# Performance work log

Measured on AMD Instinct MI355X. Metric: run time of the kernel, lower is better.

The kernel has to match this reference:

```python
import jax, jax.numpy as jnp
import numpy as np

N_NODES, N_EDGES = 100000, 800000
F_NODE, F_EDGE, N_CLASSES = 128, 16, 10


def _lin(key, fan_in, fan_out, bias=True):
    k1, k2 = jax.random.split(key)
    W = jax.random.normal(k1, (fan_in, fan_out), jnp.float32) * 0.05
    if bias:
        b = jax.random.normal(k2, (fan_out,), jnp.float32) * 0.05
        return W, b
    return (W,)


def setup_inputs() -> dict:
    key = jax.random.key(0)
    ks = jax.random.split(key, 24)
    inp = {
        "x": jax.random.normal(ks[0], (N_NODES, F_NODE), jnp.float32),
        "edge_index": jax.random.randint(ks[1], (2, N_EDGES), 0, N_NODES, jnp.int64 if jax.config.jax_enable_x64 else jnp.int32),
        "edge_attr": jax.random.normal(ks[2], (N_EDGES, F_EDGE), jnp.float32),
    }
    dims = [(F_NODE, 128), (128, 128), (128, 256)]  # (in_channels, out_channels) per layer
    i = 3
    for li, (din, dout) in enumerate(dims, start=1):
        inp[f"Wq{li}"], inp[f"bq{li}"] = _lin(ks[i], din, dout); i += 1
        inp[f"Wk{li}"], inp[f"bk{li}"] = _lin(ks[i], din, dout); i += 1
        inp[f"Wv{li}"], inp[f"bv{li}"] = _lin(ks[i], din, dout); i += 1
        (inp[f"We{li}"],) = _lin(ks[i], F_EDGE, dout, bias=False); i += 1  # PyG lin_edge: bias=False
        inp[f"Ws{li}"], inp[f"bs{li}"] = _lin(ks[i], din, dout); i += 1  # root/skip weight
    inp["Wc"], inp["bc"] = _lin(ks[i], 256, N_CLASSES)
    return inp


def transformer_conv(x, src, dst, edge_attr, Wq, bq, Wk, bk, Wv, bv, We, Ws, bs):
    """PyG TransformerConv, heads=1, concat=True, root_weight=True."""
    N = x.shape[0]
    C = Wq.shape[1]
    q = x @ Wq + bq                      # [N, C]
    k = x @ Wk + bk                      # [N, C]
    v = x @ Wv + bv                      # [N, C]
    e = edge_attr @ We                   # [E, C] edge-conditioned term
    # per-edge attention logits: <q_i, k_j + e_ij> / sqrt(C)
    alpha = jnp.sum(q[dst] * (k[src] + e), axis=-1) / jnp.sqrt(jnp.float32(C))  # [E]
    # segment softmax over edges sharing a destination node
    m = jax.ops.segment_max(alpha, dst, num_segments=N)
    p = jnp.exp(alpha - m[dst])
    s = jax.ops.segment_sum(p, dst, num_segments=N)
    a = p / (s[dst] + 1e-16)
    # scatter-aggregate weighted messages (value_j + edge term)
    out = jax.ops.segment_sum(a[:, None] * (v[src] + e), dst, num_segments=N)  # [N, C]
    return out + x @ Ws + bs             # root/skip connection


def reference(x, edge_index, edge_attr,
              Wq1, bq1, Wk1, bk1, Wv1, bv1, We1, Ws1, bs1,
              Wq2, bq2, Wk2, bk2, Wv2, bv2, We2, Ws2, bs2,
              Wq3, bq3, Wk3, bk3, Wv3, bv3, We3, Ws3, bs3,
              Wc, bc):
    src, dst = edge_index[0], edge_index[1]
    h = transformer_conv(x, src, dst, edge_attr, Wq1, bq1, Wk1, bk1, Wv1, bv1, We1, Ws1, bs1)
    h = jax.nn.relu(h)  # dropout is identity in eval mode
    h = transformer_conv(h, src, dst, edge_attr, Wq2, bq2, Wk2, bk2, Wv2, bv2, We2, Ws2, bs2)
    h = jax.nn.relu(h)
    h = transformer_conv(h, src, dst, edge_attr, Wq3, bq3, Wk3, bk3, Wv3, bv3, We3, Ws3, bs3)
    return h @ Wc + bc                   # [N, num_classes]
```

## Files before the change

### kernel.cpp

```cpp
#include <hip/hip_runtime.h>
#include <math.h>


typedef unsigned int uint;
typedef unsigned short ushort;
typedef _Float16 f16x8 __attribute__((ext_vector_type(8)));
typedef _Float16 h16x2 __attribute__((ext_vector_type(2)));
typedef float f32x4 __attribute__((ext_vector_type(4)));
typedef float f32x2 __attribute__((ext_vector_type(2)));

__device__ __forceinline__ ushort f2h(float f) {
    return __builtin_bit_cast(ushort, (_Float16)f);
}
__device__ __forceinline__ float h2f(ushort h) {
    return (float)__builtin_bit_cast(_Float16, h);
}
__device__ __forceinline__ h16x2 bch2(uint u) { return __builtin_bit_cast(h16x2, u); }
__device__ __forceinline__ f32x2 cvt2(uint u) {
    h16x2 h = bch2(u);
    return (f32x2){(float)h.x, (float)h.y};
}

#if __has_builtin(__builtin_amdgcn_fdot2)
#define FDOT2(a, b, c) __builtin_amdgcn_fdot2((a), (b), (c), false)
#else
__device__ __forceinline__ float fdot2_sw(h16x2 a, h16x2 b, float c) {
    return fmaf((float)a.x, (float)b.x, fmaf((float)a.y, (float)b.y, c));
}
#define FDOT2(a, b, c) fdot2_sw((a), (b), (c))
#endif

__global__ void k_zero(uint* p, int n) {
    int i = blockIdx.x * 256 + threadIdx.x;
    if (i < n) p[i] = 0u;
}

__global__ void k_hist(const int* __restrict__ dst, uint* __restrict__ counts, int E, int N) {
    int e = blockIdx.x * 256 + threadIdx.x;
    if (e < E) {
        int d = dst[e];
        d = (d < 0) ? 0 : (d >= N ? N - 1 : d);
        atomicAdd(&counts[d], 1u);
    }
}

__global__ void k_scan1(const uint* __restrict__ counts, uint* __restrict__ bsum, int n) {
    __shared__ uint sm[256];
    int tid = threadIdx.x;
    int base = blockIdx.x * 1024 + tid * 4;
    uint s = 0;
#pragma unroll
    for (int j = 0; j < 4; ++j)
        if (base + j < n) s += counts[base + j];
    sm[tid] = s;
    __syncthreads();
    for (int d = 128; d > 0; d >>= 1) {
        if (tid < d) sm[tid] += sm[tid + d];
        __syncthreads();
    }
    if (tid == 0) bsum[blockIdx.x] = sm[0];
}

__global__ void k_scan2(uint* bsum, int nb) {
    if (threadIdx.x == 0 && blockIdx.x == 0) {
        uint run = 0;
        for (int i = 0; i < nb; ++i) { uint v = bsum[i]; bsum[i] = run; run += v; }
    }
}

__global__ void k_scan3(const uint* __restrict__ counts, const uint* __restrict__ bsum,
                        uint* __restrict__ row_ptr, int n, int E) {
    __shared__ uint sm[256];
    int tid = threadIdx.x;
    int base = blockIdx.x * 1024 + tid * 4;
    uint local[4];
    uint s = 0;
#pragma unroll
    for (int j = 0; j < 4; ++j) {
        local[j] = (base + j < n) ? counts[base + j] : 0u;
        s += local[j];
    }
    sm[tid] = s;
    __syncthreads();
    for (int d = 1; d < 256; d <<= 1) {
        uint v = (tid >= d) ? sm[tid - d] : 0u;
        __syncthreads();
        sm[tid] += v;
        __syncthreads();
    }
    uint run = sm[tid] - s + bsum[blockIdx.x];
#pragma unroll
    for (int j = 0; j < 4; ++j)
        if (base + j < n) { row_ptr[base + j] = run; run += local[j]; }
    if (blockIdx.x == 0 && tid == 0) row_ptr[n] = (uint)E;
}

__global__ void k_fill(const int* __restrict__ ei, const uint* __restrict__ row_ptr,
                       uint* __restrict__ cursor, int2* __restrict__ srcid, int E, int N) {
    int e = blockIdx.x * 256 + threadIdx.x;
    if (e >= E) return;
    int s = ei[e];
    int d = ei[E + e];
    s = (s < 0) ? 0 : (s >= N ? N - 1 : s);
    d = (d < 0) ? 0 : (d >= N ? N - 1 : d);
    uint idx = row_ptr[d] + atomicAdd(&cursor[d], 1u);
    srcid[idx] = make_int2(s, e);
}

__global__ void k_cvt(const float4* __restrict__ in, ushort4* __restrict__ outp, int n4) {
    int i = blockIdx.x * 256 + threadIdx.x;
    if (i >= n4) return;
    float4 v = in[i];
    ushort4 o;
    o.x = f2h(v.x); o.y = f2h(v.y); o.z = f2h(v.z); o.w = f2h(v.w);
    outp[i] = o;
}

__global__ void k_packg(const float* __restrict__ Wq, const float* __restrict__ bq,
                        const float* __restrict__ We, float* __restrict__ Wgf,
                        float* __restrict__ bgf, int C) {
    int id = blockIdx.x * 256 + threadIdx.x;
    if (id < 2048) {
        int k = id >> 4, f = id & 15;
        float s = 0.f;
        for (int c = 0; c < C; ++c) s = fmaf(Wq[k * C + c], We[f * C + c], s);
        Wgf[id] = s;
    } else if (id < 2064) {
        int f = id - 2048;
        float s = 0.f;
        for (int c = 0; c < C; ++c) s = fmaf(bq[c], We[f * C + c], s);
        bgf[f] = s;
    }
}

__global__ void k_packw(const float* __restrict__ Wq, const float* __restrict__ Wk,
                        const float* __restrict__ Wv, const float* __restrict__ Ws,
                        const float* __restrict__ Wgf, ushort* __restrict__ Bp, int C) {
    int nct = (4 * C + 16) >> 4;
    int total = 4 * nct * 512;
    int id = blockIdx.x * 256 + threadIdx.x;
    if (id >= total) return;
    int j = id & 7;
    int rest = id >> 3;
    int lane = rest & 63;
    rest >>= 6;
    int ct = rest % nct;
    int kt = rest / nct;
    int k = kt * 32 + ((lane >> 4) << 3) + j;
    int c = (ct << 4) + (lane & 15);
    float w;
    if (c < 4 * C) {
        int mat = c / C, cc = c % C;
        const float* W = (mat == 0) ? Wq : (mat == 1) ? Wk : (mat == 2) ? Wv : Ws;
        w = W[k * C + cc];
    } else {
        w = Wgf[k * 16 + (c - 4 * C)];
    }
    Bp[id] = f2h(w);
}

__global__ void k_bias(const float* __restrict__ bq, const float* __restrict__ bk,
                       const float* __restrict__ bv, const float* __restrict__ bs,
                       const float* __restrict__ bgf, float* __restrict__ outp, int C) {
    int c = blockIdx.x * 256 + threadIdx.x;
    if (c >= 4 * C + 16) return;
    float v;
    if (c < 4 * C) {
        int mat = c / C, cc = c % C;
        const float* b = (mat == 0) ? bq : (mat == 1) ? bk : (mat == 2) ? bv : bs;
        v = b[cc];
    } else {
        v = bgf[c - 4 * C];
    }
    outp[c] = v;
}

__global__ __launch_bounds__(256) void k_gemm(const ushort* __restrict__ A,
                                              const ushort* __restrict__ Bp,
                                              const float* __restrict__ bias,
                                              ushort* __restrict__ H,
                                              ushort* __restrict__ S,
                                              ushort* __restrict__ g, int C) {
    int fourC = 4 * C, threeC = 3 * C;
    int P = fourC + 16;
    int nct = P >> 4;
    int lane = threadIdx.x & 63;
    int wave = threadIdx.x >> 6;
    int quad = lane >> 4;
    int r = lane & 15;
    int m0 = blockIdx.y << 4;
    int c0 = (blockIdx.x << 8) + (wave << 6);
    int ct0 = c0 >> 4;
    if (ct0 >= nct) return;
    int row = m0 + r;

    f32x4 acc[4];
#pragma unroll
    for (int i = 0; i < 4; ++i) acc[i] = (f32x4){0.f, 0.f, 0.f, 0.f};

#pragma unroll
    for (int kk = 0; kk < 4; ++kk) {
        f16x8 a = *(const f16x8*)(A + (size_t)row * 128 + kk * 32 + (quad << 3));
#pragma unroll
        for (int i = 0; i < 4; ++i) {
            if (ct0 + i < nct) {
                f16x8 b = *(const f16x8*)(Bp + ((size_t)((kk * nct + ct0 + i) << 6) + lane) * 8);
                acc[i] = __builtin_amdgcn_mfma_f32_16x16x32_f16(a, b, acc[i], 0, 0, 0);
            }
        }
    }
#pragma unroll
    for (int i = 0; i < 4; ++i) {
        int cc = c0 + (i << 4) + r;
        if (cc >= P) continue;
        float bi = bias[cc];
#pragma unroll
        for (int reg = 0; reg < 4; ++reg) {
            int rr = m0 + (quad << 2) + reg;
            ushort val = f2h(acc[i][reg] + bi);
            if (cc < threeC)      H[(size_t)rr * threeC + cc] = val;
            else if (cc < fourC)  S[(size_t)rr * C + (cc - threeC)] = val;
            else                  g[(size_t)rr * 16 + (cc - fourC)] = val;
        }
    }
}

template <int C, int GSIZE, bool RELU>
__global__ __launch_bounds__(256, 6) void k_edge(const ushort* __restrict__ H,
                                                 ushort* __restrict__ S,
                                                 const ushort* __restrict__ g,
                                                 const uint* __restrict__ row_ptr,
                                                 const int2* __restrict__ srcid,
                                                 const float* __restrict__ eattr,
                                                 const float* __restrict__ We,
                                                 int N) {
    constexpr int VR = C / GSIZE;
    constexpr int TH = 3 * C;
    constexpr int GPB = 256 / GSIZE;
    __shared__ float swex[GPB][17];
    const float scale = (C == 128) ? 0.08838834764831843f : 0.0625f;
    const float foldk = 16.0f / (float)GSIZE;

    int lane = threadIdx.x & (GSIZE - 1);
    int grp = threadIdx.x / GSIZE;
    int f = lane & 15;
    int node = blockIdx.x * GPB + grp;
    if (node >= N) return;
    int lvr = lane * VR;

    uint4 qv = *(const uint4*)(H + (size_t)node * TH + lvr);
    h16x2 q0 = bch2(qv.x), q1 = bch2(qv.y), q2 = bch2(qv.z), q3 = bch2(qv.w);
    float gl = h2f(g[(size_t)node * 16 + f]);
    float fg = foldk * gl;
    uint beg = row_ptr[node], end = row_ptr[node + 1];

    float l = 0.f, w = 0.f;
    f32x2 acc[4];
#pragma unroll
    for (int j = 0; j < 4; ++j) acc[j] = (f32x2){0.f, 0.f};

    for (uint t = beg; t < end; t += 4) {
        uint t1 = (t + 1 < end) ? t + 1 : t;
        uint t2 = (t + 2 < end) ? t + 2 : t;
        uint t3 = (t + 3 < end) ? t + 3 : t;
        int2 s0 = srcid[t], s1 = srcid[t1], s2 = srcid[t2], s3 = srcid[t3];
        float at0 = eattr[(size_t)s0.y * 16 + f];
        float at1 = eattr[(size_t)s1.y * 16 + f];
        float at2 = eattr[(size_t)s2.y * 16 + f];
        float at3 = eattr[(size_t)s3.y * 16 + f];
        const ushort* hb0 = H + (size_t)s0.x * TH + C + lvr;
        const ushort* hb1 = H + (size_t)s1.x * TH + C + lvr;
        const ushort* hb2 = H + (size_t)s2.x * TH + C + lvr;
        const ushort* hb3 = H + (size_t)s3.x * TH + C + lvr;
        uint4 k0 = *(const uint4*)hb0, v0 = *(const uint4*)(hb0 + C);
        uint4 k1 = *(const uint4*)hb1, v1 = *(const uint4*)(hb1 + C);
        uint4 k2 = *(const uint4*)hb2, v2 = *(const uint4*)(hb2 + C);
        uint4 k3 = *(const uint4*)hb3, v3 = *(const uint4*)(hb3 + C);

        float p0 = at0 * fg, p1 = at1 * fg, p2 = at2 * fg, p3 = at3 * fg;
        p0 = FDOT2(q0, bch2(k0.x), p0); p0 = FDOT2(q1, bch2(k0.y), p0);
        p0 = FDOT2(q2, bch2(k0.z), p0); p0 = FDOT2(q3, bch2(k0.w), p0);
        p1 = FDOT2(q0, bch2(k1.x), p1); p1 = FDOT2(q1, bch2(k1.y), p1);
        p1 = FDOT2(q2, bch2(k1.z), p1); p1 = FDOT2(q3, bch2(k1.w), p1);
        p2 = FDOT2(q0, bch2(k2.x), p2); p2 = FDOT2(q1, bch2(k2.y), p2);
        p2 = FDOT2(q2, bch2(k2.z), p2); p2 = FDOT2(q3, bch2(k2.w), p2);
        p3 = FDOT2(q0, bch2(k3.x), p3); p3 = FDOT2(q1, bch2(k3.y), p3);
        p3 = FDOT2(q2, bch2(k3.z), p3); p3 = FDOT2(q3, bch2(k3.w), p3);

        p0 += __shfl_xor(p0, 1); p1 += __shfl_xor(p1, 1);
        p2 += __shfl_xor(p2, 1); p3 += __shfl_xor(p3, 1);
        p0 += __shfl_xor(p0, 2); p1 += __shfl_xor(p1, 2);
        p2 += __shfl_xor(p2, 2); p3 += __shfl_xor(p3, 2);
        p0 += __shfl_xor(p0, 4); p1 += __shfl_xor(p1, 4);
        p2 += __shfl_xor(p2, 4); p3 += __shfl_xor(p3, 4);
        p0 += __shfl_xor(p0, 8); p1 += __shfl_xor(p1, 8);
        p2 += __shfl_xor(p2, 8); p3 += __shfl_xor(p3, 8);
        if (GSIZE == 32) {
            p0 += __shfl_xor(p0, 16); p1 += __shfl_xor(p1, 16);
            p2 += __shfl_xor(p2, 16); p3 += __shfl_xor(p3, 16);
        }
        float e0 = __expf(p0 * scale);
        float e1 = (t + 1 < end) ? __expf(p1 * scale) : 0.f;
        float e2 = (t + 2 < end) ? __expf(p2 * scale) : 0.f;
        float e3 = (t + 3 < end) ? __expf(p3 * scale) : 0.f;
        l += (e0 + e1) + (e2 + e3);
        w = fmaf(e0, at0, w); w = fmaf(e1, at1, w);
        w = fmaf(e2, at2, w); w = fmaf(e3, at3, w);
        f32x2 eb;
        eb = (f32x2){e0, e0};
        acc[0] = __builtin_elementwise_fma(cvt2(v0.x), eb, acc[0]);
        acc[1] = __builtin_elementwise_fma(cvt2(v0.y), eb, acc[1]);
        acc[2] = __builtin_elementwise_fma(cvt2(v0.z), eb, acc[2]);
        acc[3] = __builtin_elementwise_fma(cvt2(v0.w), eb, acc[3]);
        eb = (f32x2){e1, e1};
        acc[0] = __builtin_elementwise_fma(cvt2(v1.x), eb, acc[0]);
        acc[1] = __builtin_elementwise_fma(cvt2(v1.y), eb, acc[1]);
        acc[2] = __builtin_elementwise_fma(cvt2(v1.z), eb, acc[2]);
        acc[3] = __builtin_elementwise_fma(cvt2(v1.w), eb, acc[3]);
        eb = (f32x2){e2, e2};
        acc[0] = __builtin_elementwise_fma(cvt2(v2.x), eb, acc[0]);
        acc[1] = __builtin_elementwise_fma(cvt2(v2.y), eb, acc[1]);
        acc[2] = __builtin_elementwise_fma(cvt2(v2.z), eb, acc[2]);
        acc[3] = __builtin_elementwise_fma(cvt2(v2.w), eb, acc[3]);
        eb = (f32x2){e3, e3};
        acc[0] = __builtin_elementwise_fma(cvt2(v3.x), eb, acc[0]);
        acc[1] = __builtin_elementwise_fma(cvt2(v3.y), eb, acc[1]);
        acc[2] = __builtin_elementwise_fma(cvt2(v3.z), eb, acc[2]);
        acc[3] = __builtin_elementwise_fma(cvt2(v3.w), eb, acc[3]);
    }

    float inv = 1.f / (l + 1e-16f);
    if (lane < 16) swex[grp][lane] = w;
    f32x2 ew[4];
#pragma unroll
    for (int j = 0; j < 4; ++j) ew[j] = (f32x2){0.f, 0.f};
#pragma unroll
    for (int f2i = 0; f2i < 16; ++f2i) {
        float wfs = swex[grp][f2i];
        f32x2 wf = (f32x2){wfs, wfs};
        const f32x4* wrow = (const f32x4*)(We + f2i * C + lvr);
        f32x4 c0 = wrow[0], c1 = wrow[1];
        ew[0] = __builtin_elementwise_fma(c0.lo, wf, ew[0]);
        ew[1] = __builtin_elementwise_fma(c0.hi, wf, ew[1]);
        ew[2] = __builtin_elementwise_fma(c1.lo, wf, ew[2]);
        ew[3] = __builtin_elementwise_fma(c1.hi, wf, ew[3]);
    }
    ushort* srow = S + (size_t)node * C + lvr;
    uint4 skv = *(const uint4*)srow;
    const uint* sp = (const uint*)&skv;
    uint4 ov;
    uint* op = (uint*)&ov;
#pragma unroll
    for (int hh = 0; hh < 4; ++hh) {
        f32x2 sk = cvt2(sp[hh]);
        float o0 = (acc[hh].x + ew[hh].x) * inv + sk.x;
        float o1 = (acc[hh].y + ew[hh].y) * inv + sk.y;
        if (RELU) { o0 = fmaxf(o0, 0.f); o1 = fmaxf(o1, 0.f); }
        op[hh] = (uint)f2h(o0) | ((uint)f2h(o1) << 16);
    }
    *(uint4*)srow = ov;
}

__global__ void k_cls(const ushort* __restrict__ h, const float* __restrict__ Wc,
                      const float* __restrict__ bc, float* __restrict__ outp, int N) {
    int t = blockIdx.x * 256 + threadIdx.x;
    int node = t >> 4;
    int c = t & 15;
    if (node >= N || c >= 10) return;
    const ushort* hr = h + (size_t)node * 256;
    float acc = 0.f;
#pragma unroll 4
    for (int k4 = 0; k4 < 64; ++k4) {
        uint2 u = *(const uint2*)(hr + k4 * 4);
        f32x2 a01 = cvt2(u.x);
        f32x2 a23 = cvt2(u.y);
        int kb = k4 * 4;
        acc = fmaf(a01.x, Wc[(kb + 0) * 10 + c], acc);
        acc = fmaf(a01.y, Wc[(kb + 1) * 10 + c], acc);
        acc = fmaf(a23.x, Wc[(kb + 2) * 10 + c], acc);
        acc = fmaf(a23.y, Wc[(kb + 3) * 10 + c], acc);
    }
    outp[node * 10 + c] = acc + bc[c];
}

extern "C" void kernel_launch(void* const* d_in, const int* in_sizes, int n_in,
                              void* d_out, int out_size, void* d_ws, size_t ws_size,
                              hipStream_t stream) {
    const float* x = (const float*)d_in[0];
    const int* ei = (const int*)d_in[1];
    const float* eattr = (const float*)d_in[2];
    const int N = in_sizes[0] / 128;
    const int E = in_sizes[1] / 2;

    const float* Wq[3], *bq[3], *Wk[3], *bk[3], *Wv[3], *bv[3], *We[3], *Ws[3], *bs[3];
    for (int li = 0; li < 3; ++li) {
        int base = 3 + li * 9;
        Wq[li] = (const float*)d_in[base + 0];
        bq[li] = (const float*)d_in[base + 1];
        Wk[li] = (const float*)d_in[base + 2];
        bk[li] = (const float*)d_in[base + 3];
        Wv[li] = (const float*)d_in[base + 4];
        bv[li] = (const float*)d_in[base + 5];
        We[li] = (const float*)d_in[base + 6];
        Ws[li] = (const float*)d_in[base + 7];
        bs[li] = (const float*)d_in[base + 8];
    }
    const float* Wc = (const float*)d_in[30];
    const float* bc = (const float*)d_in[31];

    size_t off = 0;
    char* base = (char*)d_ws;
    auto alloc = [&](size_t bytes) -> void* {
        void* p = base + off;
        off = (off + bytes + 255) & ~(size_t)255;
        return p;
    };
    ushort* SA = (ushort*)alloc((size_t)N * 256 * 2);
    ushort* SB = (ushort*)alloc((size_t)N * 128 * 2);
    ushort* H  = (ushort*)alloc((size_t)N * 768 * 2);
    ushort* gbuf = (ushort*)alloc((size_t)N * 16 * 2);
    ushort* Bp = (ushort*)alloc(140000 * 2);
    float* biasc = (float*)alloc(1040 * 4);
    float* Wgf = (float*)alloc(2048 * 4);
    float* bgf = (float*)alloc(16 * 4);
    uint* row_ptr = (uint*)alloc((size_t)(N + 1) * 4);
    uint* counts = (uint*)alloc((size_t)N * 4);
    uint* cursor = (uint*)alloc((size_t)N * 4);
    uint* bsum = (uint*)alloc(1024 * 4);
    int2* srcid = (int2*)alloc((size_t)E * 8);

    ushort* xb = SB;

    int nb = (N + 1023) / 1024;

    k_zero<<<(N + 255) / 256, 256, 0, stream>>>(counts, N);
    k_zero<<<(N + 255) / 256, 256, 0, stream>>>(cursor, N);
    k_hist<<<(E + 255) / 256, 256, 0, stream>>>(ei + E, counts, E, N);
    k_scan1<<<nb, 256, 0, stream>>>(counts, bsum, N);
    k_scan2<<<1, 64, 0, stream>>>(bsum, nb);
    k_scan3<<<nb, 256, 0, stream>>>(counts, bsum, row_ptr, N, E);
    k_fill<<<(E + 255) / 256, 256, 0, stream>>>(ei, row_ptr, cursor, srcid, E, N);

    int n4 = N * 128 / 4;
    k_cvt<<<(n4 + 255) / 256, 256, 0, stream>>>((const float4*)x, (ushort4*)xb, n4);

    for (int li = 0; li < 3; ++li) {
        int C = (li == 2) ? 256 : 128;
        int P = 4 * C + 16;
        int packTotal = 4 * (P >> 4) * 512;
        const ushort* A = (li == 0) ? xb : (li == 1) ? SA : SB;
        ushort* Sout = (li == 1) ? SB : SA;

        k_packg<<<9, 256, 0, stream>>>(Wq[li], bq[li], We[li], Wgf, bgf, C);
        k_packw<<<(packTotal + 255) / 256, 256, 0, stream>>>(Wq[li], Wk[li], Wv[li], Ws[li], Wgf, Bp, C);
        k_bias<<<(P + 255) / 256, 256, 0, stream>>>(bq[li], bk[li], bv[li], bs[li], bgf, biasc, C);
        k_gemm<<<dim3((P + 255) / 256, N / 16), 256, 0, stream>>>(A, Bp, biasc, H, Sout, gbuf, C);
        if (li == 2)
            k_edge<256, 32, false><<<(N * 32 + 255) / 256, 256, 0, stream>>>(H, Sout, gbuf, row_ptr, srcid, eattr, We[li], N);
        else
            k_edge<128, 16, true><<<(N * 16 + 255) / 256, 256, 0, stream>>>(H, Sout, gbuf, row_ptr, srcid, eattr, We[li], N);
    }

    k_cls<<<(N * 16 + 255) / 256, 256, 0, stream>>>(SA, Wc, bc, (float*)d_out, N);
}
```

Before: 1.027 ms.

## Split fused edge kernel into logit/exp pass and value aggregation pass

The single per-node edge kernel becomes two passes. The first gathers K rows, computes the exponentiated attention weights, and writes them to an fp16 per-edge buffer along with the per-node denominator and edge-attr weighted sums. The second pass gathers only V rows, accumulates the weighted values and applies the edge and skip terms. The aim is to cut register pressure and per-iteration gather volume in each kernel, at the cost of an extra launch, a second index traversal, extra global traffic for the new buffers, and fp16 rounding of the weights.

```diff
diff --git a/kernel.cpp b/kernel.cpp
--- a/kernel.cpp
+++ b/kernel.cpp
@@ -225,19 +225,17 @@
     }
 }
 
-template <int C, int GSIZE, bool RELU>
-__global__ __launch_bounds__(256, 6) void k_edge(const ushort* __restrict__ H,
-                                                 ushort* __restrict__ S,
-                                                 const ushort* __restrict__ g,
-                                                 const uint* __restrict__ row_ptr,
-                                                 const int2* __restrict__ srcid,
-                                                 const float* __restrict__ eattr,
-                                                 const float* __restrict__ We,
-                                                 int N) {
+template <int C, int GSIZE>
+__global__ __launch_bounds__(256, 6) void k_edge1(const ushort* __restrict__ H,
+                                                  ushort* g,
+                                                  const uint* __restrict__ row_ptr,
+                                                  const int2* __restrict__ srcid,
+                                                  const float* __restrict__ eattr,
+                                                  ushort* __restrict__ ebuf,
+                                                  float* __restrict__ lbuf, int N) {
     constexpr int VR = C / GSIZE;
     constexpr int TH = 3 * C;
     constexpr int GPB = 256 / GSIZE;
-    __shared__ float swex[GPB][17];
     const float scale = (C == 128) ? 0.08838834764831843f : 0.0625f;
     const float foldk = 16.0f / (float)GSIZE;
 
@@ -250,32 +248,23 @@
 
     uint4 qv = *(const uint4*)(H + (size_t)node * TH + lvr);
     h16x2 q0 = bch2(qv.x), q1 = bch2(qv.y), q2 = bch2(qv.z), q3 = bch2(qv.w);
-    float gl = h2f(g[(size_t)node * 16 + f]);
-    float fg = foldk * gl;
+    float fg = foldk * h2f(g[(size_t)node * 16 + f]);
     uint beg = row_ptr[node], end = row_ptr[node + 1];
 
     float l = 0.f, w = 0.f;
-    f32x2 acc[4];
-#pragma unroll
-    for (int j = 0; j < 4; ++j) acc[j] = (f32x2){0.f, 0.f};
-
     for (uint t = beg; t < end; t += 4) {
         uint t1 = (t + 1 < end) ? t + 1 : t;
         uint t2 = (t + 2 < end) ? t + 2 : t;
         uint t3 = (t + 3 < end) ? t + 3 : t;
-        int2 s0 = srcid[t], s1 = srcid[t1], s2 = srcid[t2], s3 = srcid[t3];
-        float at0 = eattr[(size_t)s0.y * 16 + f];
-        float at1 = eattr[(size_t)s1.y * 16 + f];
-        float at2 = eattr[(size_t)s2.y * 16 + f];
-        float at3 = eattr[(size_t)s3.y * 16 + f];
-        const ushort* hb0 = H + (size_t)s0.x * TH + C + lvr;
-        const ushort* hb1 = H + (size_t)s1.x * TH + C + lvr;
-        const ushort* hb2 = H + (size_t)s2.x * TH + C + lvr;
-        const ushort* hb3 = H + (size_t)s3.x * TH + C + lvr;
-        uint4 k0 = *(const uint4*)hb0, v0 = *(const uint4*)(hb0 + C);
-        uint4 k1 = *(const uint4*)hb1, v1 = *(const uint4*)(hb1 + C);
-        uint4 k2 = *(const uint4*)hb2, v2 = *(const uint4*)(hb2 + C);
-        uint4 k3 = *(const uint4*)hb3, v3 = *(const uint4*)(hb3 + C);
+        int2 se0 = srcid[t], se1 = srcid[t1], se2 = srcid[t2], se3 = srcid[t3];
+        float at0 = eattr[(size_t)se0.y * 16 + f];
+        float at1 = eattr[(size_t)se1.y * 16 + f];
+        float at2 = eattr[(size_t)se2.y * 16 + f];
+        float at3 = eattr[(size_t)se3.y * 16 + f];
+        uint4 k0 = *(const uint4*)(H + (size_t)se0.x * TH + C + lvr);
+        uint4 k1 = *(const uint4*)(H + (size_t)se1.x * TH + C + lvr);
+        uint4 k2 = *(const uint4*)(H + (size_t)se2.x * TH + C + lvr);
+        uint4 k3 = *(const uint4*)(H + (size_t)se3.x * TH + C + lvr);
 
         float p0 = at0 * fg, p1 = at1 * fg, p2 = at2 * fg, p3 = at3 * fg;
         p0 = FDOT2(q0, bch2(k0.x), p0); p0 = FDOT2(q1, bch2(k0.y), p0);
@@ -306,6 +295,61 @@
         l += (e0 + e1) + (e2 + e3);
         w = fmaf(e0, at0, w); w = fmaf(e1, at1, w);
         w = fmaf(e2, at2, w); w = fmaf(e3, at3, w);
+        if (lane < 4) {
+            uint tj = t + lane;
+            if (tj < end) {
+                float ee = (lane == 0) ? e0 : (lane == 1) ? e1 : (lane == 2) ? e2 : e3;
+                ebuf[tj] = f2h(ee);
+            }
+        }
+    }
+    if (lane < 16) g[(size_t)node * 16 + lane] = f2h(w);
+    if (lane == 0) lbuf[node] = l;
+}
+
+template <int C, int GSIZE, bool RELU>
+__global__ __launch_bounds__(256, 6) void k_edge2(const ushort* __restrict__ H,
+                                                  ushort* __restrict__ S,
+                                                  const uint* __restrict__ row_ptr,
+                                                  const int2* __restrict__ srcid,
+                                                  const ushort* __restrict__ ebuf,
+                                                  const ushort* __restrict__ wbuf,
+                                                  const float* __restrict__ lbuf,
+                                                  const float* __restrict__ We, int N) {
+    constexpr int VR = C / GSIZE;
+    constexpr int TH = 3 * C;
+    constexpr int GPB = 256 / GSIZE;
+    __shared__ float swex[GPB][17];
+
+    int lane = threadIdx.x & (GSIZE - 1);
+    int grp = threadIdx.x / GSIZE;
+    int node = blockIdx.x * GPB + grp;
+    if (node >= N) return;
+    int lvr = lane * VR;
+    uint beg = row_ptr[node], end = row_ptr[node + 1];
+
+    ushort* srow = S + (size_t)node * C + lvr;
+    uint4 skv = *(const uint4*)srow;
+    if (lane < 16) swex[grp][lane] = h2f(wbuf[(size_t)node * 16 + lane]);
+    float l = lbuf[node];
+
+    f32x2 acc[4];
+#pragma unroll
+    for (int j = 0; j < 4; ++j) acc[j] = (f32x2){0.f, 0.f};
+
+    for (uint t = beg; t < end; t += 4) {
+        uint t1 = (t + 1 < end) ? t + 1 : t;
+        uint t2 = (t + 2 < end) ? t + 2 : t;
+        uint t3 = (t + 3 < end) ? t + 3 : t;
+        int s0 = srcid[t].x, s1 = srcid[t1].x, s2 = srcid[t2].x, s3 = srcid[t3].x;
+        float e0 = h2f(ebuf[t]);
+        float e1 = (t + 1 < end) ? h2f(ebuf[t1]) : 0.f;
+        float e2 = (t + 2 < end) ? h2f(ebuf[t2]) : 0.f;
+        float e3 = (t + 3 < end) ? h2f(ebuf[t3]) : 0.f;
+        uint4 v0 = *(const uint4*)(H + (size_t)s0 * TH + 2 * C + lvr);
+        uint4 v1 = *(const uint4*)(H + (size_t)s1 * TH + 2 * C + lvr);
+        uint4 v2 = *(const uint4*)(H + (size_t)s2 * TH + 2 * C + lvr);
+        uint4 v3 = *(const uint4*)(H + (size_t)s3 * TH + 2 * C + lvr);
         f32x2 eb;
         eb = (f32x2){e0, e0};
         acc[0] = __builtin_elementwise_fma(cvt2(v0.x), eb, acc[0]);
@@ -330,7 +374,6 @@
     }
 
     float inv = 1.f / (l + 1e-16f);
-    if (lane < 16) swex[grp][lane] = w;
     f32x2 ew[4];
 #pragma unroll
     for (int j = 0; j < 4; ++j) ew[j] = (f32x2){0.f, 0.f};
@@ -345,8 +388,6 @@
         ew[2] = __builtin_elementwise_fma(c1.lo, wf, ew[2]);
         ew[3] = __builtin_elementwise_fma(c1.hi, wf, ew[3]);
     }
-    ushort* srow = S + (size_t)node * C + lvr;
-    uint4 skv = *(const uint4*)srow;
     const uint* sp = (const uint*)&skv;
     uint4 ov;
     uint* op = (uint*)&ov;
@@ -428,8 +469,10 @@
     uint* cursor = (uint*)alloc((size_t)N * 4);
     uint* bsum = (uint*)alloc(1024 * 4);
     int2* srcid = (int2*)alloc((size_t)E * 8);
+    ushort* ebuf = (ushort*)alloc((size_t)E * 2);
 
     ushort* xb = SB;
+    float* lbuf = (float*)counts;
 
     int nb = (N + 1023) / 1024;
 
@@ -455,10 +498,13 @@
         k_packw<<<(packTotal + 255) / 256, 256, 0, stream>>>(Wq[li], Wk[li], Wv[li], Ws[li], Wgf, Bp, C);
         k_bias<<<(P + 255) / 256, 256, 0, stream>>>(bq[li], bk[li], bv[li], bs[li], bgf, biasc, C);
         k_gemm<<<dim3((P + 255) / 256, N / 16), 256, 0, stream>>>(A, Bp, biasc, H, Sout, gbuf, C);
-        if (li == 2)
-            k_edge<256, 32, false><<<(N * 32 + 255) / 256, 256, 0, stream>>>(H, Sout, gbuf, row_ptr, srcid, eattr, We[li], N);
-        else
-            k_edge<128, 16, true><<<(N * 16 + 255) / 256, 256, 0, stream>>>(H, Sout, gbuf, row_ptr, srcid, eattr, We[li], N);
+        if (li == 2) {
+            k_edge1<256, 32><<<(N * 32 + 255) / 256, 256, 0, stream>>>(H, gbuf, row_ptr, srcid, eattr, ebuf, lbuf, N);
+            k_edge2<256, 32, false><<<(N * 32 + 255) / 256, 256, 0, stream>>>(H, Sout, row_ptr, srcid, ebuf, gbuf, lbuf, We[li], N);
+        } else {
+            k_edge1<128, 16><<<(N * 16 + 255) / 256, 256, 0, stream>>>(H, gbuf, row_ptr, srcid, eattr, ebuf, lbuf, N);
+            k_edge2<128, 16, true><<<(N * 16 + 255) / 256, 256, 0, stream>>>(H, Sout, row_ptr, srcid, ebuf, gbuf, lbuf, We[li], N);
+        }
     }
 
     k_cls<<<(N * 16 + 255) / 256, 256, 0, stream>>>(SA, Wc, bc, (float*)d_out, N);
```

After: 1.054 ms. +2.7%, slower.

## Keep GEMM B fragments in registers across row tiles; unroll edge loop by two

Applied to the files above, without the earlier changes.

The GEMM kernel now loads each wave's B-weight fragments into registers once, then loops over eight 16-row tiles per block, so fewer weight fetches are repeated per block. The grid shrinks by eight in y and launch bounds request four blocks per SM. Separately, the edge aggregation loop processes two edges per iteration instead of four. This lowers register pressure and tail waste, at the cost of fewer gathers in flight to hide latency.

```diff
diff --git a/kernel.cpp b/kernel.cpp
--- a/kernel.cpp
+++ b/kernel.cpp
@@ -175,12 +175,14 @@
     outp[c] = v;
 }
 
-__global__ __launch_bounds__(256) void k_gemm(const ushort* __restrict__ A,
-                                              const ushort* __restrict__ Bp,
-                                              const float* __restrict__ bias,
-                                              ushort* __restrict__ H,
-                                              ushort* __restrict__ S,
-                                              ushort* __restrict__ g, int C) {
+__global__ __launch_bounds__(256, 4) void k_gemm(const ushort* __restrict__ A,
+                                                 const ushort* __restrict__ Bp,
+                                                 const float* __restrict__ bias,
+                                                 ushort* __restrict__ H,
+                                                 ushort* __restrict__ S,
+                                                 ushort* __restrict__ g,
+                                                 int C, int mt_total) {
+    constexpr int RT = 8;
     int fourC = 4 * C, threeC = 3 * C;
     int P = fourC + 16;
     int nct = P >> 4;
@@ -188,39 +190,61 @@
     int wave = threadIdx.x >> 6;
     int quad = lane >> 4;
     int r = lane & 15;
-    int m0 = blockIdx.y << 4;
     int c0 = (blockIdx.x << 8) + (wave << 6);
     int ct0 = c0 >> 4;
     if (ct0 >= nct) return;
-    int row = m0 + r;
-
-    f32x4 acc[4];
-#pragma unroll
-    for (int i = 0; i < 4; ++i) acc[i] = (f32x4){0.f, 0.f, 0.f, 0.f};
-
-#pragma unroll
-    for (int kk = 0; kk < 4; ++kk) {
-        f16x8 a = *(const f16x8*)(A + (size_t)row * 128 + kk * 32 + (quad << 3));
+
+    f16x8 bf[16];
+#pragma unroll
+    for (int kk = 0; kk < 4; ++kk)
 #pragma unroll
         for (int i = 0; i < 4; ++i) {
-            if (ct0 + i < nct) {
-                f16x8 b = *(const f16x8*)(Bp + ((size_t)((kk * nct + ct0 + i) << 6) + lane) * 8);
-                acc[i] = __builtin_amdgcn_mfma_f32_16x16x32_f16(a, b, acc[i], 0, 0, 0);
-            }
+            if (ct0 + i < nct)
+                bf[kk * 4 + i] = *(const f16x8*)(Bp + ((size_t)((kk * nct + ct0 + i) << 6) + lane) * 8);
+            else
+                bf[kk * 4 + i] = __builtin_bit_cast(f16x8, (uint4){0u, 0u, 0u, 0u});
         }
-    }
+
+    float bi4[4];
 #pragma unroll
     for (int i = 0; i < 4; ++i) {
         int cc = c0 + (i << 4) + r;
-        if (cc >= P) continue;
-        float bi = bias[cc];
-#pragma unroll
-        for (int reg = 0; reg < 4; ++reg) {
-            int rr = m0 + (quad << 2) + reg;
-            ushort val = f2h(acc[i][reg] + bi);
-            if (cc < threeC)      H[(size_t)rr * threeC + cc] = val;
-            else if (cc < fourC)  S[(size_t)rr * C + (cc - threeC)] = val;
-            else                  g[(size_t)rr * 16 + (cc - fourC)] = val;
+        bi4[i] = (cc < P) ? bias[cc] : 0.f;
+    }
+
+    int mt0 = blockIdx.y * RT;
+    int mt_end = mt0 + RT;
+    if (mt_end > mt_total) mt_end = mt_total;
+
+    for (int mt = mt0; mt < mt_end; ++mt) {
+        int m0 = mt << 4;
+        const ushort* arow = A + (size_t)(m0 + r) * 128 + (quad << 3);
+
+        f32x4 acc[4];
+#pragma unroll
+        for (int i = 0; i < 4; ++i) acc[i] = (f32x4){0.f, 0.f, 0.f, 0.f};
+
+#pragma unroll
+        for (int kk = 0; kk < 4; ++kk) {
+            f16x8 a = *(const f16x8*)(arow + kk * 32);
+#pragma unroll
+            for (int i = 0; i < 4; ++i)
+                if (ct0 + i < nct)
+                    acc[i] = __builtin_amdgcn_mfma_f32_16x16x32_f16(a, bf[kk * 4 + i], acc[i], 0, 0, 0);
+        }
+
+#pragma unroll
+        for (int i = 0; i < 4; ++i) {
+            int cc = c0 + (i << 4) + r;
+            if (cc >= P) continue;
+#pragma unroll
+            for (int reg = 0; reg < 4; ++reg) {
+                int rr = m0 + (quad << 2) + reg;
+                ushort val = f2h(acc[i][reg] + bi4[i]);
+                if (cc < threeC)      H[(size_t)rr * threeC + cc] = val;
+                else if (cc < fourC)  S[(size_t)rr * C + (cc - threeC)] = val;
+                else                  g[(size_t)rr * 16 + (cc - fourC)] = val;
+            }
         }
     }
 }
@@ -250,8 +274,7 @@
 
     uint4 qv = *(const uint4*)(H + (size_t)node * TH + lvr);
     h16x2 q0 = bch2(qv.x), q1 = bch2(qv.y), q2 = bch2(qv.z), q3 = bch2(qv.w);
-    float gl = h2f(g[(size_t)node * 16 + f]);
-    float fg = foldk * gl;
+    float fg = foldk * h2f(g[(size_t)node * 16 + f]);
     uint beg = row_ptr[node], end = row_ptr[node + 1];
 
     float l = 0.f, w = 0.f;
@@ -259,53 +282,34 @@
 #pragma unroll
     for (int j = 0; j < 4; ++j) acc[j] = (f32x2){0.f, 0.f};
 
-    for (uint t = beg; t < end; t += 4) {
+    for (uint t = beg; t < end; t += 2) {
         uint t1 = (t + 1 < end) ? t + 1 : t;
-        uint t2 = (t + 2 < end) ? t + 2 : t;
-        uint t3 = (t + 3 < end) ? t + 3 : t;
-        int2 s0 = srcid[t], s1 = srcid[t1], s2 = srcid[t2], s3 = srcid[t3];
-        float at0 = eattr[(size_t)s0.y * 16 + f];
-        float at1 = eattr[(size_t)s1.y * 16 + f];
-        float at2 = eattr[(size_t)s2.y * 16 + f];
-        float at3 = eattr[(size_t)s3.y * 16 + f];
-        const ushort* hb0 = H + (size_t)s0.x * TH + C + lvr;
-        const ushort* hb1 = H + (size_t)s1.x * TH + C + lvr;
-        const ushort* hb2 = H + (size_t)s2.x * TH + C + lvr;
-        const ushort* hb3 = H + (size_t)s3.x * TH + C + lvr;
+        int2 se0 = srcid[t], se1 = srcid[t1];
+        float at0 = eattr[(size_t)se0.y * 16 + f];
+        float at1 = eattr[(size_t)se1.y * 16 + f];
+        const ushort* hb0 = H + (size_t)se0.x * TH + C + lvr;
+        const ushort* hb1 = H + (size_t)se1.x * TH + C + lvr;
         uint4 k0 = *(const uint4*)hb0, v0 = *(const uint4*)(hb0 + C);
         uint4 k1 = *(const uint4*)hb1, v1 = *(const uint4*)(hb1 + C);
-        uint4 k2 = *(const uint4*)hb2, v2 = *(const uint4*)(hb2 + C);
-        uint4 k3 = *(const uint4*)hb3, v3 = *(const uint4*)(hb3 + C);
-
-        float p0 = at0 * fg, p1 = at1 * fg, p2 = at2 * fg, p3 = at3 * fg;
+
+        float p0 = at0 * fg, p1 = at1 * fg;
         p0 = FDOT2(q0, bch2(k0.x), p0); p0 = FDOT2(q1, bch2(k0.y), p0);
         p0 = FDOT2(q2, bch2(k0.z), p0); p0 = FDOT2(q3, bch2(k0.w), p0);
         p1 = FDOT2(q0, bch2(k1.x), p1); p1 = FDOT2(q1, bch2(k1.y), p1);
         p1 = FDOT2(q2, bch2(k1.z), p1); p1 = FDOT2(q3, bch2(k1.w), p1);
-        p2 = FDOT2(q0, bch2(k2.x), p2); p2 = FDOT2(q1, bch2(k2.y), p2);
-        p2 = FDOT2(q2, bch2(k2.z), p2); p2 = FDOT2(q3, bch2(k2.w), p2);
-        p3 = FDOT2(q0, bch2(k3.x), p3); p3 = FDOT2(q1, bch2(k3.y), p3);
-        p3 = FDOT2(q2, bch2(k3.z), p3); p3 = FDOT2(q3, bch2(k3.w), p3);
 
         p0 += __shfl_xor(p0, 1); p1 += __shfl_xor(p1, 1);
-        p2 += __shfl_xor(p2, 1); p3 += __shfl_xor(p3, 1);
         p0 += __shfl_xor(p0, 2); p1 += __shfl_xor(p1, 2);
-        p2 += __shfl_xor(p2, 2); p3 += __shfl_xor(p3, 2);
         p0 += __shfl_xor(p0, 4); p1 += __shfl_xor(p1, 4);
-        p2 += __shfl_xor(p2, 4); p3 += __shfl_xor(p3, 4);
         p0 += __shfl_xor(p0, 8); p1 += __shfl_xor(p1, 8);
-        p2 += __shfl_xor(p2, 8); p3 += __shfl_xor(p3, 8);
         if (GSIZE == 32) {
             p0 += __shfl_xor(p0, 16); p1 += __shfl_xor(p1, 16);
-            p2 += __shfl_xor(p2, 16); p3 += __shfl_xor(p3, 16);
         }
         float e0 = __expf(p0 * scale);
         float e1 = (t + 1 < end) ? __expf(p1 * scale) : 0.f;
-        float e2 = (t + 2 < end) ? __expf(p2 * scale) : 0.f;
-        float e3 = (t + 3 < end) ? __expf(p3 * scale) : 0.f;
-        l += (e0 + e1) + (e2 + e3);
-        w = fmaf(e0, at0, w); w = fmaf(e1, at1, w);
-        w = fmaf(e2, at2, w); w = fmaf(e3, at3, w);
+        l += e0 + e1;
+        w = fmaf(e0, at0, w);
+        w = fmaf(e1, at1, w);
         f32x2 eb;
         eb = (f32x2){e0, e0};
         acc[0] = __builtin_elementwise_fma(cvt2(v0.x), eb, acc[0]);
@@ -317,16 +321,6 @@
         acc[1] = __builtin_elementwise_fma(cvt2(v1.y), eb, acc[1]);
         acc[2] = __builtin_elementwise_fma(cvt2(v1.z), eb, acc[2]);
         acc[3] = __builtin_elementwise_fma(cvt2(v1.w), eb, acc[3]);
-        eb = (f32x2){e2, e2};
-        acc[0] = __builtin_elementwise_fma(cvt2(v2.x), eb, acc[0]);
-        acc[1] = __builtin_elementwise_fma(cvt2(v2.y), eb, acc[1]);
-        acc[2] = __builtin_elementwise_fma(cvt2(v2.z), eb, acc[2]);
-        acc[3] = __builtin_elementwise_fma(cvt2(v2.w), eb, acc[3]);
-        eb = (f32x2){e3, e3};
-        acc[0] = __builtin_elementwise_fma(cvt2(v3.x), eb, acc[0]);
-        acc[1] = __builtin_elementwise_fma(cvt2(v3.y), eb, acc[1]);
-        acc[2] = __builtin_elementwise_fma(cvt2(v3.z), eb, acc[2]);
-        acc[3] = __builtin_elementwise_fma(cvt2(v3.w), eb, acc[3]);
     }
 
     float inv = 1.f / (l + 1e-16f);
@@ -444,6 +438,7 @@
     int n4 = N * 128 / 4;
     k_cvt<<<(n4 + 255) / 256, 256, 0, stream>>>((const float4*)x, (ushort4*)xb, n4);
 
+    int mt_total = N / 16;
     for (int li = 0; li < 3; ++li) {
         int C = (li == 2) ? 256 : 128;
         int P = 4 * C + 16;
@@ -454,7 +449,7 @@
         k_packg<<<9, 256, 0, stream>>>(Wq[li], bq[li], We[li], Wgf, bgf, C);
         k_packw<<<(packTotal + 255) / 256, 256, 0, stream>>>(Wq[li], Wk[li], Wv[li], Ws[li], Wgf, Bp, C);
         k_bias<<<(P + 255) / 256, 256, 0, stream>>>(bq[li], bk[li], bv[li], bs[li], bgf, biasc, C);
-        k_gemm<<<dim3((P + 255) / 256, N / 16), 256, 0, stream>>>(A, Bp, biasc, H, Sout, gbuf, C);
+        k_gemm<<<dim3((P + 255) / 256, (mt_total + 7) / 8), 256, 0, stream>>>(A, Bp, biasc, H, Sout, gbuf, C, mt_total);
         if (li == 2)
             k_edge<256, 32, false><<<(N * 32 + 255) / 256, 256, 0, stream>>>(H, Sout, gbuf, row_ptr, srcid, eattr, We[li], N);
         else
```

After: 944.7 us. 8.0% less time.
